# Kernel tuning notes

Measured on AMD Instinct MI355X. Metric: run time of the kernel, lower is better.

Reference implementation:

```python
import jax, jax.numpy as jnp
import numpy as np
from jax import lax

B_, N_, DIM, HID, DST, NT, IR, DTR, HH, WW = 16, 4096, 192, 384, 16, 17, 128, 24, 64, 64


def _selective_scan(u, delta, A, Bs, Cs, D, delta_bias):
    # u, delta: (B, Din, L); A: (Din, N); Bs, Cs: (B, N, L); D, delta_bias: (Din,)
    delta = jax.nn.softplus(delta + delta_bias[None, :, None])
    dT = jnp.moveaxis(delta, 2, 0)   # (L, B, Din)
    uT = jnp.moveaxis(u, 2, 0)       # (L, B, Din)
    BT = jnp.moveaxis(Bs, 2, 0)      # (L, B, N)
    CT = jnp.moveaxis(Cs, 2, 0)      # (L, B, N)
    Bsz, Din, L = u.shape
    Nst = A.shape[1]
    h0 = jnp.zeros((Bsz, Din, Nst), u.dtype)

    def step(h, inp):
        d_l, u_l, b_l, c_l = inp
        da = jnp.exp(d_l[:, :, None] * A[None])              # (B, Din, N)
        h = da * h + (d_l * u_l)[:, :, None] * b_l[:, None, :]
        y = jnp.einsum('bdn,bn->bd', h, c_l)
        return h, y

    _, ys = lax.scan(step, h0, (dT, uT, BT, CT))
    y = jnp.moveaxis(ys, 0, 2)                               # (B, Din, L)
    return y + u * D[None, :, None]


def _assm_forward(x, token_weight, gumbel_noise, embB, route_w1, route_b1, route_w2,
                  route_b2, inproj_w, inproj_b, cpe_w, cpe_b, x_proj_w, dt_w, dt_b,
                  A_logs, Ds, norm_g, norm_b, outproj_w, outproj_b, H, W, gather_type):
    B, n, C = x.shape
    hidden = inproj_w.shape[0]
    dst = token_weight.shape[1]
    dtr = dt_w.shape[1]

    # routing + gumbel-softmax (hard, straight-through)
    full_emb = embB @ token_weight                           # (NT, d_state)
    hmid = jax.nn.gelu(x @ route_w1.T + route_b1)
    logits = jax.nn.log_softmax(hmid @ route_w2.T + route_b2, axis=-1)
    y_soft = jax.nn.softmax(logits + gumbel_noise, axis=-1)
    idx = jnp.argmax(y_soft, axis=-1)                        # (B, n)
    y_hard = jax.nn.one_hot(idx, logits.shape[-1], dtype=y_soft.dtype)
    cls_policy = y_hard + y_soft - lax.stop_gradient(y_soft)
    prompt = cls_policy @ full_emb                           # (B, n, d_state)

    det = lax.stop_gradient(idx)
    # (gather_type 3/5 keypoint-group remap omitted: gather_type == 1 here)
    sort_idx = jnp.argsort(det, axis=-1)                     # (B, n)
    inv_idx = jnp.argsort(sort_idx, axis=-1)                 # index_reverse

    # in_proj (1x1 conv == pointwise linear) then depthwise CPE gate
    xi = x @ inproj_w.T + inproj_b                           # (B, n, hidden)
    xg = xi.reshape(B, H, W, hidden).transpose(0, 3, 1, 2)   # NCHW
    cpe = lax.conv_general_dilated(xg, cpe_w, (1, 1), 'SAME',
                                   feature_group_count=hidden,
                                   dimension_numbers=('NCHW', 'OIHW', 'NCHW'))
    cpe = cpe + cpe_b[None, :, None, None]
    xg = xg * jax.nn.sigmoid(cpe)
    xflat = xg.reshape(B, hidden, n).transpose(0, 2, 1)      # (B, n, hidden)

    sem_x = jnp.take_along_axis(xflat, sort_idx[:, :, None], axis=1)

    # Selective_Scan core
    xs = sem_x.transpose(0, 2, 1)                            # (B, Din, L)
    x_dbl = jnp.einsum('bdl,cd->bcl', xs, x_proj_w)          # (B, dtr+2N, L)
    dts, Bs, Cs = jnp.split(x_dbl, [dtr, dtr + dst], axis=1)
    dts = jnp.einsum('brl,dr->bdl', dts, dt_w)
    if gather_type != 0:
        Cs = Cs + prompt.transpose(0, 2, 1)
    A = -jnp.exp(A_logs)
    y = _selective_scan(xs, dts, A, Bs, Cs, Ds, dt_b)        # (B, Din, L)
    y = y.transpose(0, 2, 1)                                 # (B, L, hidden)

    mu = jnp.mean(y, axis=-1, keepdims=True)
    var = jnp.mean(jnp.square(y - mu), axis=-1, keepdims=True)
    yn = (y - mu) / jnp.sqrt(var + 1e-5) * norm_g + norm_b
    out = yn @ outproj_w.T + outproj_b                       # (B, n, dim)
    out = jnp.take_along_axis(out, inv_idx[:, :, None], axis=1)
    return out


def setup_inputs() -> dict:
    key = jax.random.key(0)
    ks = jax.random.split(key, 16)

    def rn(k, sh, s=0.02):
        return jax.random.normal(k, sh, dtype=jnp.float32) * s

    u = jax.random.uniform(ks[0], (B_, N_, NT), jnp.float32, 1e-6, 1.0 - 1e-6)
    gumbel = -jnp.log(-jnp.log(u))

    # faithful dt bias init (inverse-softplus of log-uniform dt)
    rng = np.random.default_rng(0)
    dt = np.exp(rng.uniform(size=HID) * (np.log(0.1) - np.log(0.001)) + np.log(0.001))
    dt = np.clip(dt, 1e-4, None)
    inv_dt = dt + np.log(-np.expm1(-dt))

    A_logs = jnp.log(jnp.tile(jnp.arange(1, DST + 1, dtype=jnp.float32), (HID, 1)))

    return {
        'x': jax.random.normal(ks[1], (B_, N_, DIM), jnp.float32),
        'token_weight': rn(ks[2], (IR, DST), 0.1),
        'gumbel_noise': gumbel,
        'embB': jax.random.uniform(ks[3], (NT, IR), jnp.float32, -1.0 / NT, 1.0 / NT),
        'route_w1': rn(ks[4], (DIM // 3, DIM)),
        'route_b1': jnp.zeros((DIM // 3,), jnp.float32),
        'route_w2': rn(ks[5], (NT, DIM // 3)),
        'route_b2': jnp.zeros((NT,), jnp.float32),
        'inproj_w': rn(ks[6], (HID, DIM)),
        'inproj_b': jnp.zeros((HID,), jnp.float32),
        'cpe_w': rn(ks[7], (HID, 1, 3, 3), 0.1),
        'cpe_b': jnp.zeros((HID,), jnp.float32),
        'x_proj_w': rn(ks[8], (DTR + 2 * DST, HID)),
        'dt_w': jax.random.uniform(ks[9], (HID, DTR), jnp.float32, -DTR ** -0.5, DTR ** -0.5),
        'dt_b': jnp.asarray(inv_dt, jnp.float32),
        'A_logs': A_logs,
        'Ds': jnp.ones((HID,), jnp.float32),
        'norm_g': jnp.ones((HID,), jnp.float32),
        'norm_b': jnp.zeros((HID,), jnp.float32),
        'outproj_w': rn(ks[10], (DIM, HID)),
        'outproj_b': jnp.zeros((DIM,), jnp.float32),
        'H': HH,
        'W': WW,
        'gather_type': 1,
    }


def reference(x, token_weight, gumbel_noise, embB, route_w1, route_b1, route_w2,
              route_b2, inproj_w, inproj_b, cpe_w, cpe_b, x_proj_w, dt_w, dt_b,
              A_logs, Ds, norm_g, norm_b, outproj_w, outproj_b, H, W, gather_type):
    return _assm_forward(x, token_weight, gumbel_noise, embB, route_w1, route_b1,
                         route_w2, route_b2, inproj_w, inproj_b, cpe_w, cpe_b,
                         x_proj_w, dt_w, dt_b, A_logs, Ds, norm_g, norm_b,
                         outproj_w, outproj_b, H, W, gather_type)
```

## Files before the change

kernel.cpp:

```cpp
#include <hip/hip_runtime.h>
#include <math.h>

#define NB 16
#define NL 4096
#define ND 192
#define NH 384
#define NS 16
#define NTK 17
#define NIR 128
#define NR 24
#define NHH 64
#define NWW 64
#define NCHUNKS 32
#define CHUNKLEN 128
#define NTOK (NB*NL)

typedef __attribute__((ext_vector_type(8))) short short8;
typedef __attribute__((ext_vector_type(4))) float floatx4;

__device__ __forceinline__ float gelu_tanh(float x){
  return 0.5f*x*(1.0f + tanhf(0.7978845608028654f*(x + 0.044715f*x*x*x)));
}
__device__ __forceinline__ float softplus_f(float x){
  return (x > 20.0f) ? x : log1pf(expf(x));
}
__device__ __forceinline__ short f2bf(float f){
  unsigned u = __float_as_uint(f);
  unsigned r = (u + 0x7fffu + ((u >> 16) & 1u)) >> 16;
  return (short)r;
}

union Pack8 { uint4 v; short s[8]; };

__global__ void k_emb(const float* __restrict__ embB, const float* __restrict__ tw,
                      float* __restrict__ fe){
  for (int o = threadIdx.x; o < NTK*NS; o += 256){
    int t = o / NS, s = o % NS;
    float acc = 0.f;
    for (int i = 0; i < NIR; ++i) acc += embB[t*NIR+i]*tw[i*NS+s];
    fe[o] = acc;
  }
}

__global__ void k_cvtw(const float* __restrict__ inw, const float* __restrict__ ow,
                       const float* __restrict__ xpw, const float* __restrict__ dtw,
                       short* __restrict__ inwb, short* __restrict__ owb,
                       short* __restrict__ xpwb, short* __restrict__ dtwb){
  int i = blockIdx.x*256 + threadIdx.x;
  int stride = gridDim.x*256;
  for (int p = i; p < NH*ND; p += stride) inwb[p] = f2bf(inw[p]);
  for (int p = i; p < ND*NH; p += stride) owb[p] = f2bf(ow[p]);
  for (int p = i; p < 56*NH; p += stride) xpwb[p] = f2bf(xpw[p]);
  for (int p = i; p < NH*32; p += stride){
    int r = p >> 5, c = p & 31;
    dtwb[p] = (c < NR) ? f2bf(dtw[r*NR + c]) : (short)0;
  }
}

template<int EPI>
__global__ __launch_bounds__(256) void k_gemm(const float* __restrict__ A, int lda,
    const float* __restrict__ W, int ldw, const float* __restrict__ bias,
    float* __restrict__ C, int ldc, int N, int K){
  __shared__ float As[16][68];
  __shared__ float Ws[16][68];
  int tid = threadIdx.x;
  int m0 = blockIdx.x*64, n0 = blockIdx.y*64;
  int tx = tid & 15, ty = tid >> 4;
  int srow = tid >> 2, skseg = (tid & 3)*4;
  float acc[4][4] = {};
  for (int k0 = 0; k0 < K; k0 += 16){
    {
      const float* ap = A + (size_t)(m0+srow)*lda + k0 + skseg;
      float4 v = *(const float4*)ap;
      As[skseg+0][srow]=v.x; As[skseg+1][srow]=v.y;
      As[skseg+2][srow]=v.z; As[skseg+3][srow]=v.w;
    }
    {
      float4 v = {0.f,0.f,0.f,0.f};
      if (n0 + srow < N) v = *(const float4*)(W + (size_t)(n0+srow)*ldw + k0 + skseg);
      Ws[skseg+0][srow]=v.x; Ws[skseg+1][srow]=v.y;
      Ws[skseg+2][srow]=v.z; Ws[skseg+3][srow]=v.w;
    }
    __syncthreads();
    #pragma unroll
    for (int kk = 0; kk < 16; ++kk){
      float4 av = *(const float4*)&As[kk][ty*4];
      float4 wv = *(const float4*)&Ws[kk][tx*4];
      acc[0][0] += av.x*wv.x; acc[0][1] += av.x*wv.y;
      acc[0][2] += av.x*wv.z; acc[0][3] += av.x*wv.w;
      acc[1][0] += av.y*wv.x; acc[1][1] += av.y*wv.y;
      acc[1][2] += av.y*wv.z; acc[1][3] += av.y*wv.w;
      acc[2][0] += av.z*wv.x; acc[2][1] += av.z*wv.y;
      acc[2][2] += av.z*wv.z; acc[2][3] += av.z*wv.w;
      acc[3][0] += av.w*wv.x; acc[3][1] += av.w*wv.y;
      acc[3][2] += av.w*wv.z; acc[3][3] += av.w*wv.w;
    }
    __syncthreads();
  }
  #pragma unroll
  for (int i = 0; i < 4; ++i){
    int m = m0 + ty*4 + i;
    #pragma unroll
    for (int j = 0; j < 4; ++j){
      int n = n0 + tx*4 + j;
      if (n < N){
        float v = acc[i][j] + (bias ? bias[n] : 0.f);
        if (EPI==1) v = gelu_tanh(v);
        C[(size_t)m*ldc + n] = v;
      }
    }
  }
}

template<int EPI, int AF32, int LNA>
__global__ __launch_bounds__(256) void k_mfma(const void* __restrict__ Aptr, int lda,
    const short* __restrict__ Wbf, int ldw, const float* __restrict__ bias,
    float* __restrict__ C, int ldc, int N, int K, const int* __restrict__ remap,
    const float* __restrict__ lnm, const float* __restrict__ lnr,
    const float* __restrict__ lng, const float* __restrict__ lnb){
  __shared__ short As[128*40];
  __shared__ short Bs[64*40];
  int tid = threadIdx.x;
  int m0 = blockIdx.x*128, n0 = blockIdx.y*64;
  int w = tid >> 6, lane = tid & 63;
  int lq = lane >> 4, lr = lane & 15;
  floatx4 acc[2][4];
  #pragma unroll
  for (int i = 0; i < 2; ++i)
    #pragma unroll
    for (int j = 0; j < 4; ++j) acc[i][j] = (floatx4){0.f,0.f,0.f,0.f};
  int ar = tid >> 1, aq = (tid & 1)*2;
  int br = tid >> 2, bq = tid & 3;
  float mr = 0.f, rr = 0.f;
  if (LNA){ mr = lnm[m0+ar]; rr = lnr[m0+ar]; }
  for (int k0 = 0; k0 < K; k0 += 32){
    Pack8 sa0, sa1;
    if (AF32){
      const float* ap = (const float*)Aptr + (size_t)(m0+ar)*lda + k0 + aq*8;
      float f[16];
      float4 f0 = *(const float4*)(ap);
      float4 f1 = *(const float4*)(ap+4);
      float4 f2 = *(const float4*)(ap+8);
      float4 f3 = *(const float4*)(ap+12);
      f[0]=f0.x; f[1]=f0.y; f[2]=f0.z; f[3]=f0.w;
      f[4]=f1.x; f[5]=f1.y; f[6]=f1.z; f[7]=f1.w;
      f[8]=f2.x; f[9]=f2.y; f[10]=f2.z; f[11]=f2.w;
      f[12]=f3.x; f[13]=f3.y; f[14]=f3.z; f[15]=f3.w;
      if (LNA){
        const float* gp = lng + k0 + aq*8;
        const float* bp = lnb + k0 + aq*8;
        #pragma unroll
        for (int j = 0; j < 16; ++j) f[j] = (f[j]-mr)*rr*gp[j] + bp[j];
      }
      #pragma unroll
      for (int j = 0; j < 8; ++j){ sa0.s[j] = f2bf(f[j]); sa1.s[j] = f2bf(f[8+j]); }
    } else {
      const short* ap = (const short*)Aptr + (size_t)(m0+ar)*lda + k0 + aq*8;
      sa0.v = *(const uint4*)ap;
      sa1.v = *(const uint4*)(ap + 8);
    }
    uint4 bv = {0u,0u,0u,0u};
    if (n0 + br < N) bv = *(const uint4*)(Wbf + (size_t)(n0+br)*ldw + k0 + bq*8);
    __syncthreads();
    *(uint4*)&As[ar*40 + aq*8]     = sa0.v;
    *(uint4*)&As[ar*40 + aq*8 + 8] = sa1.v;
    *(uint4*)&Bs[br*40 + bq*8]     = bv;
    __syncthreads();
    short8 a0 = *(const short8*)&As[(w*32      + lr)*40 + lq*8];
    short8 a1 = *(const short8*)&As[(w*32 + 16 + lr)*40 + lq*8];
    short8 b0 = *(const short8*)&Bs[(     lr)*40 + lq*8];
    short8 b1 = *(const short8*)&Bs[(16 + lr)*40 + lq*8];
    short8 b2 = *(const short8*)&Bs[(32 + lr)*40 + lq*8];
    short8 b3 = *(const short8*)&Bs[(48 + lr)*40 + lq*8];
    acc[0][0] = __builtin_amdgcn_mfma_f32_16x16x32_bf16(a0, b0, acc[0][0], 0,0,0);
    acc[0][1] = __builtin_amdgcn_mfma_f32_16x16x32_bf16(a0, b1, acc[0][1], 0,0,0);
    acc[0][2] = __builtin_amdgcn_mfma_f32_16x16x32_bf16(a0, b2, acc[0][2], 0,0,0);
    acc[0][3] = __builtin_amdgcn_mfma_f32_16x16x32_bf16(a0, b3, acc[0][3], 0,0,0);
    acc[1][0] = __builtin_amdgcn_mfma_f32_16x16x32_bf16(a1, b0, acc[1][0], 0,0,0);
    acc[1][1] = __builtin_amdgcn_mfma_f32_16x16x32_bf16(a1, b1, acc[1][1], 0,0,0);
    acc[1][2] = __builtin_amdgcn_mfma_f32_16x16x32_bf16(a1, b2, acc[1][2], 0,0,0);
    acc[1][3] = __builtin_amdgcn_mfma_f32_16x16x32_bf16(a1, b3, acc[1][3], 0,0,0);
  }
  #pragma unroll
  for (int mt = 0; mt < 2; ++mt){
    #pragma unroll
    for (int r = 0; r < 4; ++r){
      int m = m0 + w*32 + mt*16 + lq*4 + r;
      int orow = (EPI==3) ? remap[m] : m;
      #pragma unroll
      for (int nt = 0; nt < 4; ++nt){
        int n = n0 + nt*16 + lr;
        if (n < N){
          float v = acc[mt][nt][r] + (bias ? bias[n] : 0.f);
          if (EPI==2) v = softplus_f(v);
          C[(size_t)orow*ldc + n] = v;
        }
      }
    }
  }
}

__global__ __launch_bounds__(256) void k_argmax(const float* __restrict__ hmid,
    const float* __restrict__ w2, const float* __restrict__ b2,
    const float* __restrict__ gumbel, int* __restrict__ idx){
  int g = blockIdx.x*256 + threadIdx.x;
  float hm[64];
  const float4* hp = (const float4*)(hmid + (size_t)g*64);
  #pragma unroll
  for (int i = 0; i < 16; ++i){
    float4 v = hp[i];
    hm[i*4+0]=v.x; hm[i*4+1]=v.y; hm[i*4+2]=v.z; hm[i*4+3]=v.w;
  }
  float best = -INFINITY; int bi = 0;
  for (int c = 0; c < NTK; ++c){
    float s = b2[c] + gumbel[(size_t)g*NTK + c];
    #pragma unroll
    for (int j = 0; j < 64; ++j) s += hm[j]*w2[c*64+j];
    if (s > best){ best = s; bi = c; }
  }
  idx[g] = bi;
}

__global__ __launch_bounds__(256) void k_sort(const int* __restrict__ idx,
    int* __restrict__ rmap, int* __restrict__ inv){
  int b = blockIdx.x, t = threadIdx.x;
  __shared__ int hist[NTK][256];
  __shared__ int tot[NTK];
  __shared__ int keybase[NTK];
  int keys[16];
  const int* ip = idx + b*NL + t*16;
  #pragma unroll
  for (int i = 0; i < 16; ++i) keys[i] = ip[i];
  #pragma unroll
  for (int k = 0; k < NTK; ++k){
    int c = 0;
    #pragma unroll
    for (int i = 0; i < 16; ++i) c += (keys[i]==k) ? 1 : 0;
    hist[k][t] = c;
  }
  __syncthreads();
  if (t < NTK){
    int run = 0;
    for (int j = 0; j < 256; ++j){ int v = hist[t][j]; hist[t][j] = run; run += v; }
    tot[t] = run;
  }
  __syncthreads();
  if (t == 0){
    int base = 0;
    for (int k = 0; k < NTK; ++k){ keybase[k] = base; base += tot[k]; }
  }
  __syncthreads();
  #pragma unroll
  for (int i = 0; i < 16; ++i){
    int k = keys[i];
    int cb = 0;
    #pragma unroll
    for (int j = 0; j < 16; ++j) cb += (j < i && keys[j]==k) ? 1 : 0;
    int pos = keybase[k] + hist[k][t] + cb;
    rmap[b*NL + pos] = b*NL + t*16 + i;
    inv[b*NL + t*16 + i] = pos;
  }
}

__global__ __launch_bounds__(384) void k_cpe(const float* __restrict__ xi,
    const float* __restrict__ cw, const float* __restrict__ cb,
    const int* __restrict__ inv, float* __restrict__ us){
  int bl = blockIdx.x;
  int cg = bl & 3;
  int xt = (bl>>2) & 7;
  int yt = (bl>>5) & 7;
  int b  = bl >> 8;
  __shared__ float tile[10*10*96];
  int tx = threadIdx.x;
  int ty = threadIdx.y;
  int c0 = cg*96;
  int ch = c0 + tx;
  for (int yy = 0; yy < 10; ++yy){
    int gy = yt*8 + yy - 1;
    for (int xx = ty; xx < 10; xx += 4){
      int gx = xt*8 + xx - 1;
      float v = 0.f;
      if (gy >= 0 && gy < NHH && gx >= 0 && gx < NWW)
        v = xi[((size_t)(b*NL + gy*NWW + gx))*NH + ch];
      tile[(yy*10 + xx)*96 + tx] = v;
    }
  }
  float wreg[9];
  #pragma unroll
  for (int j = 0; j < 9; ++j) wreg[j] = cw[ch*9 + j];
  float bias = cb[ch];
  __syncthreads();
  for (int yy = ty; yy < 8; yy += 4){
    #pragma unroll
    for (int xx = 0; xx < 8; ++xx){
      float acc = bias;
      #pragma unroll
      for (int dy = 0; dy < 3; ++dy)
        #pragma unroll
        for (int dx = 0; dx < 3; ++dx)
          acc += tile[((yy+dy)*10 + (xx+dx))*96 + tx] * wreg[dy*3+dx];
      float center = tile[((yy+1)*10 + (xx+1))*96 + tx];
      float gate = 1.f/(1.f + expf(-acc));
      int l = (yt*8+yy)*NWW + xt*8+xx;
      int pos = inv[b*NL + l];
      us[((size_t)(b*NL + pos))*NH + ch] = center*gate;
    }
  }
}

__global__ __launch_bounds__(256) void k_bc(const float* __restrict__ dbl,
    const int* __restrict__ idx, const float* __restrict__ fe,
    const int* __restrict__ gt, float* __restrict__ Bsb, float* __restrict__ Csb,
    short* __restrict__ dtsb){
  int g = blockIdx.x*256 + threadIdx.x;
  const float* dr = dbl + (size_t)g*56;
  int id = idx[g];
  int gather = gt[0];
  #pragma unroll
  for (int n = 0; n < NR; ++n) dtsb[(size_t)g*32 + n] = f2bf(dr[n]);
  #pragma unroll
  for (int n = NR; n < 32; ++n) dtsb[(size_t)g*32 + n] = 0;
  #pragma unroll
  for (int n = 0; n < NS; ++n){
    Bsb[(size_t)g*NS + n] = dr[24+n];
    float c = dr[40+n];
    if (gather != 0) c += fe[id*NS + n];
    Csb[(size_t)g*NS + n] = c;
  }
}

__device__ __forceinline__ void decay16(bool pw, float dlt, const float* An, float* a){
  if (pw){
    float r  = __expf(dlt*An[0]);
    float r2 = r*r;
    float r3 = r2*r;
    float r4 = r2*r2;
    float r8 = r4*r4;
    float r12 = r8*r4;
    a[0]=r;     a[1]=r2;     a[2]=r3;     a[3]=r4;
    a[4]=r4*r;  a[5]=r4*r2;  a[6]=r4*r3;  a[7]=r8;
    a[8]=r8*r;  a[9]=r8*r2;  a[10]=r8*r3; a[11]=r12;
    a[12]=r12*r; a[13]=r12*r2; a[14]=r12*r3; a[15]=r8*r8;
  } else {
    #pragma unroll
    for (int n = 0; n < NS; ++n) a[n] = __expf(dlt*An[n]);
  }
}
__device__ __forceinline__ bool pwcheck(const float* An){
  bool pw = true;
  #pragma unroll
  for (int n = 1; n < NS; ++n)
    pw = pw && (fabsf(An[n] - (n+1)*An[0]) <= 1e-4f*fabsf(An[n]));
  return pw;
}

__global__ __launch_bounds__(384) void k_scan1(const float* __restrict__ delta,
    const float* __restrict__ us, const float* __restrict__ Bsb,
    const float* __restrict__ A_logs, float* __restrict__ Aprod, float* __restrict__ Boff){
  int bc = blockIdx.x;
  int c = bc & (NCHUNKS-1);
  int b = bc >> 5;
  int d = threadIdx.x;
  __shared__ float4 Bsh[CHUNKLEN*4];
  int base = b*NL + c*CHUNKLEN;
  {
    const float4* Bg = (const float4*)(Bsb + (size_t)base*NS);
    for (int p = d; p < CHUNKLEN*4; p += 384) Bsh[p] = Bg[p];
  }
  float An[NS];
  #pragma unroll
  for (int n = 0; n < NS; ++n) An[n] = -expf(A_logs[d*NS + n]);
  bool pw = pwcheck(An);
  float h[NS];
  #pragma unroll
  for (int n = 0; n < NS; ++n) h[n]=0.f;
  float sd = 0.f;
  __syncthreads();
  size_t gi = (size_t)base*NH + d;
  float dlt = delta[gi];
  float uv  = us[gi];
  #pragma unroll 2
  for (int s = 0; s < CHUNKLEN; ++s){
    float dltc = dlt, uvc = uv;
    if (s < CHUNKLEN-1){
      dlt = delta[gi + NH];
      uv  = us[gi + NH];
    }
    float du = dltc*uvc;
    sd += dltc;
    float a[NS];
    decay16(pw, dltc, An, a);
    float bb[NS];
    #pragma unroll
    for (int q = 0; q < 4; ++q) *(float4*)&bb[4*q] = Bsh[s*4 + q];
    #pragma unroll
    for (int n = 0; n < NS; ++n) h[n] = a[n]*h[n] + du*bb[n];
    gi += NH;
  }
  float ap[NS];
  decay16(pw, sd, An, ap);
  size_t o = ((size_t)bc*NH + d)*NS;
  #pragma unroll
  for (int n = 0; n < NS; ++n){ Aprod[o+n]=ap[n]; Boff[o+n]=h[n]; }
}

__global__ __launch_bounds__(256) void k_scan2(const float* __restrict__ Aprod,
    float* __restrict__ Boff){
  int i = blockIdx.x*256 + threadIdx.x;
  int dn = i % (NH*NS);
  int b = i / (NH*NS);
  float h = 0.f;
  for (int c = 0; c < NCHUNKS; ++c){
    size_t o = ((size_t)(b*NCHUNKS + c)*NH*NS) + dn;
    float a = Aprod[o];
    float bo = Boff[o];
    Boff[o] = h;
    h = a*h + bo;
  }
}

__global__ __launch_bounds__(384) void k_scan3(const float* __restrict__ delta,
    const float* __restrict__ Bsb, const float* __restrict__ Csb,
    const float* __restrict__ A_logs, const float* __restrict__ Ds,
    const float* __restrict__ hinit, float* __restrict__ us){
  int bc = blockIdx.x;
  int c = bc & (NCHUNKS-1);
  int b = bc >> 5;
  int d = threadIdx.x;
  __shared__ float4 Bsh[CHUNKLEN*4];
  __shared__ float4 Csh[CHUNKLEN*4];
  int base = b*NL + c*CHUNKLEN;
  {
    const float4* Bg = (const float4*)(Bsb + (size_t)base*NS);
    const float4* Cg = (const float4*)(Csb + (size_t)base*NS);
    for (int p = d; p < CHUNKLEN*4; p += 384){
      Bsh[p] = Bg[p];
      Csh[p] = Cg[p];
    }
  }
  float An[NS];
  #pragma unroll
  for (int n = 0; n < NS; ++n) An[n] = -expf(A_logs[d*NS + n]);
  bool pw = pwcheck(An);
  float h[NS];
  size_t ho = ((size_t)bc*NH + d)*NS;
  #pragma unroll
  for (int n = 0; n < NS; ++n) h[n] = hinit[ho + n];
  float Dd = Ds[d];
  __syncthreads();
  size_t gi = (size_t)base*NH + d;
  float dlt = delta[gi];
  float uv  = us[gi];
  #pragma unroll 2
  for (int s = 0; s < CHUNKLEN; ++s){
    float dltc = dlt, uvc = uv;
    if (s < CHUNKLEN-1){
      dlt = delta[gi + NH];
      uv  = us[gi + NH];
    }
    float du = dltc*uvc;
    float a[NS];
    decay16(pw, dltc, An, a);
    float bb[NS], cc[NS];
    #pragma unroll
    for (int q = 0; q < 4; ++q){
      *(float4*)&bb[4*q] = Bsh[s*4 + q];
      *(float4*)&cc[4*q] = Csh[s*4 + q];
    }
    float y = 0.f;
    #pragma unroll
    for (int n = 0; n < NS; ++n){
      h[n] = a[n]*h[n] + du*bb[n];
      y += h[n]*cc[n];
    }
    us[gi] = y + uvc*Dd;
    gi += NH;
  }
}

__global__ __launch_bounds__(256) void k_lnstat(const float* __restrict__ y,
    float* __restrict__ mean, float* __restrict__ rstd){
  int g = blockIdx.x*4 + (threadIdx.x >> 6);
  int lane = threadIdx.x & 63;
  size_t ro = (size_t)g*NH;
  float v[6];
  #pragma unroll
  for (int i = 0; i < 6; ++i) v[i] = y[ro + i*64 + lane];
  float s = 0.f;
  #pragma unroll
  for (int i = 0; i < 6; ++i) s += v[i];
  #pragma unroll
  for (int off = 32; off > 0; off >>= 1) s += __shfl_xor(s, off);
  float mu = s * (1.f/NH);
  float vs = 0.f;
  #pragma unroll
  for (int i = 0; i < 6; ++i){ float d = v[i]-mu; vs += d*d; }
  #pragma unroll
  for (int off = 32; off > 0; off >>= 1) vs += __shfl_xor(vs, off);
  float rs = rsqrtf(vs*(1.f/NH) + 1e-5f);
  if (lane == 0){ mean[g] = mu; rstd[g] = rs; }
}

extern "C" void kernel_launch(void* const* d_in, const int* in_sizes, int n_in,
                              void* d_out, int out_size, void* d_ws, size_t ws_size,
                              hipStream_t stream){
  const float* x      = (const float*)d_in[0];
  const float* tw     = (const float*)d_in[1];
  const float* gumbel = (const float*)d_in[2];
  const float* embB   = (const float*)d_in[3];
  const float* rw1    = (const float*)d_in[4];
  const float* rb1    = (const float*)d_in[5];
  const float* rw2    = (const float*)d_in[6];
  const float* rb2    = (const float*)d_in[7];
  const float* inw    = (const float*)d_in[8];
  const float* inb    = (const float*)d_in[9];
  const float* cw     = (const float*)d_in[10];
  const float* cb     = (const float*)d_in[11];
  const float* xpw    = (const float*)d_in[12];
  const float* dtw    = (const float*)d_in[13];
  const float* dtb    = (const float*)d_in[14];
  const float* A_logs = (const float*)d_in[15];
  const float* Ds     = (const float*)d_in[16];
  const float* ng     = (const float*)d_in[17];
  const float* nbv    = (const float*)d_in[18];
  const float* ow     = (const float*)d_in[19];
  const float* ob     = (const float*)d_in[20];
  const int*   gt     = (const int*)d_in[23];
  float* out = (float*)d_out;

  float* ws = (float*)d_ws;
  size_t o = 0;
  float* fe   = ws + o; o += 512;
  int* idx    = (int*)(ws + o); o += NTOK;
  int* rmap   = (int*)(ws + o); o += NTOK;
  int* inv    = (int*)(ws + o); o += NTOK;
  float* hmid = ws + o; o += (size_t)NTOK*64;
  float* xi   = ws + o; o += (size_t)NTOK*NH;
  float* us   = ws + o; o += (size_t)NTOK*NH;
  float* Bsb  = ws + o; o += (size_t)NTOK*NS;
  float* Csb  = ws + o; o += (size_t)NTOK*NS;
  float* Apr  = ws + o; o += (size_t)NB*NCHUNKS*NH*NS;
  float* Bof  = ws + o; o += (size_t)NB*NCHUNKS*NH*NS;
  short* inwb = (short*)(ws + o); o += (NH*ND)/2;
  short* owb  = (short*)(ws + o); o += (ND*NH)/2;
  short* xpwb = (short*)(ws + o); o += (56*NH)/2 + 32;
  short* dtwb = (short*)(ws + o); o += (NH*32)/2;
  float* dbl = hmid;
  float* delta = xi;
  short* dtsb = (short*)Apr;
  float* lnmean = (float*)idx;
  float* lnrstd = (float*)inv;

  k_emb<<<1,256,0,stream>>>(embB, tw, fe);
  k_cvtw<<<64,256,0,stream>>>(inw, ow, xpw, dtw, inwb, owb, xpwb, dtwb);
  k_gemm<1><<<dim3(NTOK/64,1),256,0,stream>>>(x, ND, rw1, ND, rb1, hmid, 64, 64, ND);
  k_argmax<<<NTOK/256,256,0,stream>>>(hmid, rw2, rb2, gumbel, idx);
  k_sort<<<NB,256,0,stream>>>(idx, rmap, inv);
  k_mfma<0,1,0><<<dim3(NTOK/128,6),256,0,stream>>>(x, ND, inwb, ND, inb, xi, NH, NH, ND,
      nullptr, nullptr, nullptr, nullptr, nullptr);
  k_cpe<<<NB*64*4,dim3(96,4),0,stream>>>(xi, cw, cb, inv, us);
  k_mfma<0,1,0><<<dim3(NTOK/128,1),256,0,stream>>>(us, NH, xpwb, NH, nullptr, dbl, 56, 56, NH,
      nullptr, nullptr, nullptr, nullptr, nullptr);
  k_bc<<<NTOK/256,256,0,stream>>>(dbl, idx, fe, gt, Bsb, Csb, dtsb);
  k_mfma<2,0,0><<<dim3(NTOK/128,6),256,0,stream>>>(dtsb, 32, dtwb, 32, dtb, delta, NH, NH, 32,
      nullptr, nullptr, nullptr, nullptr, nullptr);
  k_scan1<<<NB*NCHUNKS,384,0,stream>>>(delta, us, Bsb, A_logs, Apr, Bof);
  k_scan2<<<(NB*NH*NS)/256,256,0,stream>>>(Apr, Bof);
  k_scan3<<<NB*NCHUNKS,384,0,stream>>>(delta, Bsb, Csb, A_logs, Ds, Bof, us);
  k_lnstat<<<NTOK/4,256,0,stream>>>(us, lnmean, lnrstd);
  k_mfma<3,1,1><<<dim3(NTOK/128,3),256,0,stream>>>(us, NH, owb, NH, ob, out, ND, ND, NH,
      rmap, lnmean, lnrstd, ng, nbv);
}
```

Before: 733.5 us.

## Split scan state across two threads per channel with shuffle-reduced output

The chunked selective-scan kernels now use two threads per channel, each holding 8 of the 16 state elements, so blocks grow from 384 to 768 threads. The output dot product is combined with a lane shuffle, and delta and u are prefetched four steps ahead instead of one. This aims to raise occupancy and hide latency in the scan kernels, which were limited by register use and a serial dependency. The cost is duplicated delta/u loads, duplicated exp work in the non-power path, and an extra shuffle on every step.

```diff
diff --git a/kernel.cpp b/kernel.cpp
--- a/kernel.cpp
+++ b/kernel.cpp
@@ -329,79 +329,102 @@
   }
 }
 
-__device__ __forceinline__ void decay16(bool pw, float dlt, const float* An, float* a){
+__device__ __forceinline__ bool pwsetup(const float* __restrict__ A_logs, int d,
+                                        float& An0){
+  float a0 = -expf(A_logs[d*NS]);
+  An0 = a0;
+  bool pw = true;
+  #pragma unroll
+  for (int n = 1; n < NS; ++n){
+    float v = -expf(A_logs[d*NS + n]);
+    pw = pw && (fabsf(v - (n+1)*a0) <= 1e-4f*fabsf(v));
+  }
+  return pw;
+}
+
+__device__ __forceinline__ void decay8(bool pw, float dlt, float An0,
+                                       const float* __restrict__ Alp, int half,
+                                       float* a){
   if (pw){
-    float r  = __expf(dlt*An[0]);
+    float r  = __expf(dlt*An0);
     float r2 = r*r;
-    float r3 = r2*r;
     float r4 = r2*r2;
     float r8 = r4*r4;
-    float r12 = r8*r4;
-    a[0]=r;     a[1]=r2;     a[2]=r3;     a[3]=r4;
-    a[4]=r4*r;  a[5]=r4*r2;  a[6]=r4*r3;  a[7]=r8;
-    a[8]=r8*r;  a[9]=r8*r2;  a[10]=r8*r3; a[11]=r12;
-    a[12]=r12*r; a[13]=r12*r2; a[14]=r12*r3; a[15]=r8*r8;
+    float bse = half ? r8 : 1.f;
+    a[0] = bse*r;
+    a[1] = bse*r2;
+    a[2] = a[1]*r;
+    a[3] = bse*r4;
+    a[4] = a[3]*r;
+    a[5] = a[3]*r2;
+    a[6] = a[5]*r;
+    a[7] = bse*r8;
   } else {
     #pragma unroll
-    for (int n = 0; n < NS; ++n) a[n] = __expf(dlt*An[n]);
-  }
-}
-__device__ __forceinline__ bool pwcheck(const float* An){
-  bool pw = true;
-  #pragma unroll
-  for (int n = 1; n < NS; ++n)
-    pw = pw && (fabsf(An[n] - (n+1)*An[0]) <= 1e-4f*fabsf(An[n]));
-  return pw;
-}
-
-__global__ __launch_bounds__(384) void k_scan1(const float* __restrict__ delta,
+    for (int j = 0; j < 8; ++j) a[j] = __expf(dlt * (-expf(Alp[j])));
+  }
+}
+
+__global__ __launch_bounds__(768, 6) void k_scan1(const float* __restrict__ delta,
     const float* __restrict__ us, const float* __restrict__ Bsb,
     const float* __restrict__ A_logs, float* __restrict__ Aprod, float* __restrict__ Boff){
   int bc = blockIdx.x;
   int c = bc & (NCHUNKS-1);
   int b = bc >> 5;
-  int d = threadIdx.x;
+  int tid = threadIdx.x;
+  int d = tid >> 1, half = tid & 1;
   __shared__ float4 Bsh[CHUNKLEN*4];
   int base = b*NL + c*CHUNKLEN;
   {
     const float4* Bg = (const float4*)(Bsb + (size_t)base*NS);
-    for (int p = d; p < CHUNKLEN*4; p += 384) Bsh[p] = Bg[p];
-  }
-  float An[NS];
-  #pragma unroll
-  for (int n = 0; n < NS; ++n) An[n] = -expf(A_logs[d*NS + n]);
-  bool pw = pwcheck(An);
-  float h[NS];
-  #pragma unroll
-  for (int n = 0; n < NS; ++n) h[n]=0.f;
+    for (int p = tid; p < CHUNKLEN*4; p += 768) Bsh[p] = Bg[p];
+  }
+  float An0;
+  bool pw = pwsetup(A_logs, d, An0);
+  const float* Alp = A_logs + d*NS + half*8;
+  float h[8];
+  #pragma unroll
+  for (int n = 0; n < 8; ++n) h[n] = 0.f;
   float sd = 0.f;
   __syncthreads();
-  size_t gi = (size_t)base*NH + d;
-  float dlt = delta[gi];
-  float uv  = us[gi];
-  #pragma unroll 2
-  for (int s = 0; s < CHUNKLEN; ++s){
-    float dltc = dlt, uvc = uv;
-    if (s < CHUNKLEN-1){
-      dlt = delta[gi + NH];
-      uv  = us[gi + NH];
-    }
-    float du = dltc*uvc;
-    sd += dltc;
-    float a[NS];
-    decay16(pw, dltc, An, a);
-    float bb[NS];
-    #pragma unroll
-    for (int q = 0; q < 4; ++q) *(float4*)&bb[4*q] = Bsh[s*4 + q];
-    #pragma unroll
-    for (int n = 0; n < NS; ++n) h[n] = a[n]*h[n] + du*bb[n];
-    gi += NH;
-  }
-  float ap[NS];
-  decay16(pw, sd, An, ap);
-  size_t o = ((size_t)bc*NH + d)*NS;
-  #pragma unroll
-  for (int n = 0; n < NS; ++n){ Aprod[o+n]=ap[n]; Boff[o+n]=h[n]; }
+  const float* dp = delta + (size_t)base*NH + d;
+  const float* up = us    + (size_t)base*NH + d;
+  float pd[4], pu[4];
+  #pragma unroll
+  for (int j = 0; j < 4; ++j){ pd[j] = dp[(size_t)j*NH]; pu[j] = up[(size_t)j*NH]; }
+  const float* dln = dp + (size_t)4*NH;
+  const float* uln = up + (size_t)4*NH;
+  int bq = half*2;
+  for (int s = 0; s < CHUNKLEN; s += 4){
+    bool pf = (s + 4) < CHUNKLEN;
+    #pragma unroll
+    for (int jj = 0; jj < 4; ++jj){
+      float dltc = pd[jj], uvc = pu[jj];
+      if (pf){ pd[jj] = dln[(size_t)jj*NH]; pu[jj] = uln[(size_t)jj*NH]; }
+      float du = dltc*uvc;
+      sd += dltc;
+      float a[8];
+      decay8(pw, dltc, An0, Alp, half, a);
+      float4 b0 = Bsh[(s+jj)*4 + bq];
+      float4 b1 = Bsh[(s+jj)*4 + bq + 1];
+      h[0] = a[0]*h[0] + du*b0.x;
+      h[1] = a[1]*h[1] + du*b0.y;
+      h[2] = a[2]*h[2] + du*b0.z;
+      h[3] = a[3]*h[3] + du*b0.w;
+      h[4] = a[4]*h[4] + du*b1.x;
+      h[5] = a[5]*h[5] + du*b1.y;
+      h[6] = a[6]*h[6] + du*b1.z;
+      h[7] = a[7]*h[7] + du*b1.w;
+    }
+    dln += 4*NH; uln += 4*NH;
+  }
+  float ap[8];
+  decay8(pw, sd, An0, Alp, half, ap);
+  size_t o = ((size_t)bc*NH + d)*NS + half*8;
+  *(float4*)(Aprod + o)     = make_float4(ap[0],ap[1],ap[2],ap[3]);
+  *(float4*)(Aprod + o + 4) = make_float4(ap[4],ap[5],ap[6],ap[7]);
+  *(float4*)(Boff + o)      = make_float4(h[0],h[1],h[2],h[3]);
+  *(float4*)(Boff + o + 4)  = make_float4(h[4],h[5],h[6],h[7]);
 }
 
 __global__ __launch_bounds__(256) void k_scan2(const float* __restrict__ Aprod,
@@ -419,62 +442,78 @@
   }
 }
 
-__global__ __launch_bounds__(384) void k_scan3(const float* __restrict__ delta,
+__global__ __launch_bounds__(768, 6) void k_scan3(const float* __restrict__ delta,
     const float* __restrict__ Bsb, const float* __restrict__ Csb,
     const float* __restrict__ A_logs, const float* __restrict__ Ds,
     const float* __restrict__ hinit, float* __restrict__ us){
   int bc = blockIdx.x;
   int c = bc & (NCHUNKS-1);
   int b = bc >> 5;
-  int d = threadIdx.x;
+  int tid = threadIdx.x;
+  int d = tid >> 1, half = tid & 1;
   __shared__ float4 Bsh[CHUNKLEN*4];
   __shared__ float4 Csh[CHUNKLEN*4];
   int base = b*NL + c*CHUNKLEN;
   {
     const float4* Bg = (const float4*)(Bsb + (size_t)base*NS);
     const float4* Cg = (const float4*)(Csb + (size_t)base*NS);
-    for (int p = d; p < CHUNKLEN*4; p += 384){
+    for (int p = tid; p < CHUNKLEN*4; p += 768){
       Bsh[p] = Bg[p];
       Csh[p] = Cg[p];
     }
   }
-  float An[NS];
-  #pragma unroll
-  for (int n = 0; n < NS; ++n) An[n] = -expf(A_logs[d*NS + n]);
-  bool pw = pwcheck(An);
-  float h[NS];
-  size_t ho = ((size_t)bc*NH + d)*NS;
-  #pragma unroll
-  for (int n = 0; n < NS; ++n) h[n] = hinit[ho + n];
+  float An0;
+  bool pw = pwsetup(A_logs, d, An0);
+  const float* Alp = A_logs + d*NS + half*8;
+  float h[8];
+  size_t ho = ((size_t)bc*NH + d)*NS + half*8;
+  {
+    float4 h0 = *(const float4*)(hinit + ho);
+    float4 h1 = *(const float4*)(hinit + ho + 4);
+    h[0]=h0.x; h[1]=h0.y; h[2]=h0.z; h[3]=h0.w;
+    h[4]=h1.x; h[5]=h1.y; h[6]=h1.z; h[7]=h1.w;
+  }
   float Dd = Ds[d];
   __syncthreads();
-  size_t gi = (size_t)base*NH + d;
-  float dlt = delta[gi];
-  float uv  = us[gi];
-  #pragma unroll 2
-  for (int s = 0; s < CHUNKLEN; ++s){
-    float dltc = dlt, uvc = uv;
-    if (s < CHUNKLEN-1){
-      dlt = delta[gi + NH];
-      uv  = us[gi + NH];
-    }
-    float du = dltc*uvc;
-    float a[NS];
-    decay16(pw, dltc, An, a);
-    float bb[NS], cc[NS];
-    #pragma unroll
-    for (int q = 0; q < 4; ++q){
-      *(float4*)&bb[4*q] = Bsh[s*4 + q];
-      *(float4*)&cc[4*q] = Csh[s*4 + q];
-    }
-    float y = 0.f;
-    #pragma unroll
-    for (int n = 0; n < NS; ++n){
-      h[n] = a[n]*h[n] + du*bb[n];
-      y += h[n]*cc[n];
-    }
-    us[gi] = y + uvc*Dd;
-    gi += NH;
+  const float* dp = delta + (size_t)base*NH + d;
+  float* up = us + (size_t)base*NH + d;
+  float pd[4], pu[4];
+  #pragma unroll
+  for (int j = 0; j < 4; ++j){ pd[j] = dp[(size_t)j*NH]; pu[j] = up[(size_t)j*NH]; }
+  const float* dln = dp + (size_t)4*NH;
+  const float* uln = up + (size_t)4*NH;
+  float* usw = up;
+  int bq = half*2;
+  for (int s = 0; s < CHUNKLEN; s += 4){
+    bool pf = (s + 4) < CHUNKLEN;
+    #pragma unroll
+    for (int jj = 0; jj < 4; ++jj){
+      float dltc = pd[jj], uvc = pu[jj];
+      if (pf){ pd[jj] = dln[(size_t)jj*NH]; pu[jj] = uln[(size_t)jj*NH]; }
+      float du = dltc*uvc;
+      float a[8];
+      decay8(pw, dltc, An0, Alp, half, a);
+      float4 b0 = Bsh[(s+jj)*4 + bq];
+      float4 b1 = Bsh[(s+jj)*4 + bq + 1];
+      float4 c0 = Csh[(s+jj)*4 + bq];
+      float4 c1 = Csh[(s+jj)*4 + bq + 1];
+      h[0] = a[0]*h[0] + du*b0.x;
+      h[1] = a[1]*h[1] + du*b0.y;
+      h[2] = a[2]*h[2] + du*b0.z;
+      h[3] = a[3]*h[3] + du*b0.w;
+      h[4] = a[4]*h[4] + du*b1.x;
+      h[5] = a[5]*h[5] + du*b1.y;
+      h[6] = a[6]*h[6] + du*b1.z;
+      h[7] = a[7]*h[7] + du*b1.w;
+      float y0 = h[0]*c0.x + h[1]*c0.y;
+      float y1 = h[2]*c0.z + h[3]*c0.w;
+      float y2 = h[4]*c1.x + h[5]*c1.y;
+      float y3 = h[6]*c1.z + h[7]*c1.w;
+      float y = (y0+y1) + (y2+y3);
+      float yt = y + __shfl_xor(y, 1);
+      if (!half) usw[(size_t)jj*NH] = yt + uvc*Dd;
+    }
+    dln += 4*NH; uln += 4*NH; usw += 4*NH;
   }
 }
 
@@ -564,9 +603,9 @@
   k_bc<<<NTOK/256,256,0,stream>>>(dbl, idx, fe, gt, Bsb, Csb, dtsb);
   k_mfma<2,0,0><<<dim3(NTOK/128,6),256,0,stream>>>(dtsb, 32, dtwb, 32, dtb, delta, NH, NH, 32,
       nullptr, nullptr, nullptr, nullptr, nullptr);
-  k_scan1<<<NB*NCHUNKS,384,0,stream>>>(delta, us, Bsb, A_logs, Apr, Bof);
+  k_scan1<<<NB*NCHUNKS,768,0,stream>>>(delta, us, Bsb, A_logs, Apr, Bof);
   k_scan2<<<(NB*NH*NS)/256,256,0,stream>>>(Apr, Bof);
-  k_scan3<<<NB*NCHUNKS,384,0,stream>>>(delta, Bsb, Csb, A_logs, Ds, Bof, us);
+  k_scan3<<<NB*NCHUNKS,768,0,stream>>>(delta, Bsb, Csb, A_logs, Ds, Bof, us);
   k_lnstat<<<NTOK/4,256,0,stream>>>(us, lnmean, lnrstd);
   k_mfma<3,1,1><<<dim3(NTOK/128,3),256,0,stream>>>(us, NH, owb, NH, ob, out, ND, ND, NH,
       rmap, lnmean, lnrstd, ng, nbv);
```

Result: slower. 833.5 us (+13.6%).

## Halve scan chunk length and recompute chunk decay from summed delta

Applied to the files above, without the earlier changes.

Doubles the number of scan chunks (64 chunks of 64 steps), giving k_scan1/k_scan3 twice as many blocks on the GPU and half the serial length per block. Instead of storing a full per-state decay product array, k_scan1 writes only the summed delta per channel and k_scan2 recomputes the decay with exp, which cuts workspace traffic. The dtsb staging buffer now aliases Bof. k_scan3's output dot product is split into four partial sums to shorten the dependency chain. The cost is a longer sequential loop in k_scan2 and extra exp calls there.

```diff
diff --git a/kernel.cpp b/kernel.cpp
--- a/kernel.cpp
+++ b/kernel.cpp
@@ -11,8 +11,8 @@
 #define NR 24
 #define NHH 64
 #define NWW 64
-#define NCHUNKS 32
-#define CHUNKLEN 128
+#define NCHUNKS 64
+#define CHUNKLEN 64
 #define NTOK (NB*NL)
 
 typedef __attribute__((ext_vector_type(8))) short short8;
@@ -356,10 +356,10 @@
 
 __global__ __launch_bounds__(384) void k_scan1(const float* __restrict__ delta,
     const float* __restrict__ us, const float* __restrict__ Bsb,
-    const float* __restrict__ A_logs, float* __restrict__ Aprod, float* __restrict__ Boff){
+    const float* __restrict__ A_logs, float* __restrict__ sds, float* __restrict__ Boff){
   int bc = blockIdx.x;
   int c = bc & (NCHUNKS-1);
-  int b = bc >> 5;
+  int b = bc >> 6;
   int d = threadIdx.x;
   __shared__ float4 Bsh[CHUNKLEN*4];
   int base = b*NL + c*CHUNKLEN;
@@ -397,22 +397,24 @@
     for (int n = 0; n < NS; ++n) h[n] = a[n]*h[n] + du*bb[n];
     gi += NH;
   }
-  float ap[NS];
-  decay16(pw, sd, An, ap);
+  sds[(size_t)bc*NH + d] = sd;
   size_t o = ((size_t)bc*NH + d)*NS;
   #pragma unroll
-  for (int n = 0; n < NS; ++n){ Aprod[o+n]=ap[n]; Boff[o+n]=h[n]; }
-}
-
-__global__ __launch_bounds__(256) void k_scan2(const float* __restrict__ Aprod,
-    float* __restrict__ Boff){
+  for (int n = 0; n < NS; ++n) Boff[o+n] = h[n];
+}
+
+__global__ __launch_bounds__(256) void k_scan2(const float* __restrict__ A_logs,
+    const float* __restrict__ sds, float* __restrict__ Boff){
   int i = blockIdx.x*256 + threadIdx.x;
   int dn = i % (NH*NS);
   int b = i / (NH*NS);
+  float An = -expf(A_logs[dn]);
   float h = 0.f;
   for (int c = 0; c < NCHUNKS; ++c){
-    size_t o = ((size_t)(b*NCHUNKS + c)*NH*NS) + dn;
-    float a = Aprod[o];
+    int bc = b*NCHUNKS + c;
+    float sd = sds[(size_t)bc*NH + (dn >> 4)];
+    float a = __expf(sd*An);
+    size_t o = (size_t)bc*(NH*NS) + dn;
     float bo = Boff[o];
     Boff[o] = h;
     h = a*h + bo;
@@ -425,7 +427,7 @@
     const float* __restrict__ hinit, float* __restrict__ us){
   int bc = blockIdx.x;
   int c = bc & (NCHUNKS-1);
-  int b = bc >> 5;
+  int b = bc >> 6;
   int d = threadIdx.x;
   __shared__ float4 Bsh[CHUNKLEN*4];
   __shared__ float4 Csh[CHUNKLEN*4];
@@ -467,12 +469,17 @@
       *(float4*)&bb[4*q] = Bsh[s*4 + q];
       *(float4*)&cc[4*q] = Csh[s*4 + q];
     }
-    float y = 0.f;
-    #pragma unroll
-    for (int n = 0; n < NS; ++n){
-      h[n] = a[n]*h[n] + du*bb[n];
-      y += h[n]*cc[n];
-    }
+    #pragma unroll
+    for (int n = 0; n < NS; ++n) h[n] = a[n]*h[n] + du*bb[n];
+    float ya = 0.f, yb = 0.f, yc = 0.f, yd = 0.f;
+    #pragma unroll
+    for (int q = 0; q < 4; ++q){
+      ya += h[q]*cc[q];
+      yb += h[4+q]*cc[4+q];
+      yc += h[8+q]*cc[8+q];
+      yd += h[12+q]*cc[12+q];
+    }
+    float y = (ya+yb)+(yc+yd);
     us[gi] = y + uvc*Dd;
     gi += NH;
   }
@@ -539,7 +546,7 @@
   float* us   = ws + o; o += (size_t)NTOK*NH;
   float* Bsb  = ws + o; o += (size_t)NTOK*NS;
   float* Csb  = ws + o; o += (size_t)NTOK*NS;
-  float* Apr  = ws + o; o += (size_t)NB*NCHUNKS*NH*NS;
+  float* sds  = ws + o; o += (size_t)NB*NCHUNKS*NH;
   float* Bof  = ws + o; o += (size_t)NB*NCHUNKS*NH*NS;
   short* inwb = (short*)(ws + o); o += (NH*ND)/2;
   short* owb  = (short*)(ws + o); o += (ND*NH)/2;
@@ -547,7 +554,7 @@
   short* dtwb = (short*)(ws + o); o += (NH*32)/2;
   float* dbl = hmid;
   float* delta = xi;
-  short* dtsb = (short*)Apr;
+  short* dtsb = (short*)Bof;
   float* lnmean = (float*)idx;
   float* lnrstd = (float*)inv;
 
@@ -564,8 +571,8 @@
   k_bc<<<NTOK/256,256,0,stream>>>(dbl, idx, fe, gt, Bsb, Csb, dtsb);
   k_mfma<2,0,0><<<dim3(NTOK/128,6),256,0,stream>>>(dtsb, 32, dtwb, 32, dtb, delta, NH, NH, 32,
       nullptr, nullptr, nullptr, nullptr, nullptr);
-  k_scan1<<<NB*NCHUNKS,384,0,stream>>>(delta, us, Bsb, A_logs, Apr, Bof);
-  k_scan2<<<(NB*NH*NS)/256,256,0,stream>>>(Apr, Bof);
+  k_scan1<<<NB*NCHUNKS,384,0,stream>>>(delta, us, Bsb, A_logs, sds, Bof);
+  k_scan2<<<(NB*NH*NS)/256,256,0,stream>>>(A_logs, sds, Bof);
   k_scan3<<<NB*NCHUNKS,384,0,stream>>>(delta, Bsb, Csb, A_logs, Ds, Bof, us);
   k_lnstat<<<NTOK/4,256,0,stream>>>(us, lnmean, lnrstd);
   k_mfma<3,1,1><<<dim3(NTOK/128,3),256,0,stream>>>(us, NH, owb, NH, ob, out, ND, ND, NH,
```

Result: no change. 747.3 us (+1.9%).
